# Performance work log

Hardware: AMD Instinct MI355X
Metric: run time of the kernel (lower is better)

## Reference

```python
import jax, jax.numpy as jnp
import numpy as np

N, K, C = 100000, 32, 128  # n_nodes, max_degree, channels


def setup_inputs() -> dict:
    key = jax.random.key(0)
    k1, k2, k3, k4 = jax.random.split(key, 4)
    x = jax.random.normal(k1, (N, C), dtype=jnp.float32)
    edge_index = jax.random.randint(k2, (N, K), 0, N, dtype=jnp.int64)
    # GCNConv uses nn.Linear(in, out, bias=False): weight shape [out, in]
    W1 = jax.random.normal(k3, (C, C), dtype=jnp.float32) / np.sqrt(C)
    W2 = jax.random.normal(k4, (C, C), dtype=jnp.float32) / np.sqrt(C)
    return {"x": x, "edge_index": edge_index, "W1": W1, "W2": W2}


def _gcn_layer(x, edge_index, W):
    # node degree counts valid (>=0) neighbors plus self
    deg = jnp.sum(edge_index >= 0, axis=-1, keepdims=True).astype(x.dtype) + 1.0
    sqrt_deg = jnp.sqrt(deg)
    h = (x @ W.T) / sqrt_deg  # [N, C]
    # pad with a zero row so index -1 (padding) gathers zeros
    padded = jnp.concatenate([h, jnp.zeros((1, h.shape[-1]), h.dtype)], axis=0)
    neigh_sum = padded[edge_index].sum(axis=1)  # [N, K, C] -> [N, C]
    return (neigh_sum + h) / sqrt_deg


def reference(x, edge_index, W1, W2):
    h = jax.nn.elu(_gcn_layer(x, edge_index, W1))
    h = jax.nn.elu(_gcn_layer(h, edge_index, W2))
    return h
```

## Files before the change

### kernel.cpp

```cpp
#include <hip/hip_runtime.h>
#include <hip/hip_bf16.h>
#include <math.h>

namespace {

constexpr int C = 128;
constexpr int K = 32;

typedef float float4v __attribute__((ext_vector_type(4)));
typedef short short8v __attribute__((ext_vector_type(8)));
typedef unsigned short ushort8v __attribute__((ext_vector_type(8)));
typedef int int2v __attribute__((ext_vector_type(2)));

__device__ __forceinline__ float bf2f(unsigned short u) {
    return __uint_as_float(((unsigned int)u) << 16);
}
__device__ __forceinline__ unsigned short f2bf(float x) {
    __hip_bfloat16 h = __float2bfloat16(x);
    return *(unsigned short*)&h;
}

__global__ __launch_bounds__(256) void deg_kernel(
    const int* __restrict__ edge, float* __restrict__ invs,
    unsigned int* __restrict__ hzero, const float* __restrict__ W1,
    const float* __restrict__ W2, unsigned short* __restrict__ whl, int N) {
    const int bid = blockIdx.x;
    const int t = threadIdx.x;

    if (bid == 0 && t < 64) {
        hzero[(size_t)N * (C / 2) + t] = 0u;
    }
    if (bid >= 1 && bid <= 128) {
        int which = (bid - 1) >> 6;
        int p = ((bid - 1) & 63) * 256 + t;
        float w = (which ? W2 : W1)[p];
        unsigned short hb = f2bf(w);
        unsigned short lb = f2bf(w - bf2f(hb));
        unsigned short* dst = whl + (size_t)which * 32768;
        dst[p] = hb;
        dst[16384 + p] = lb;
    }

    int node = bid * 32 + (t >> 3);
    int k4 = (t & 7) * 4;
    int4 e = make_int4(-1, -1, -1, -1);
    if (node < N) e = *(const int4*)(edge + (size_t)node * K + k4);
    int cnt = (e.x >= 0) + (e.y >= 0) + (e.z >= 0) + (e.w >= 0);
    cnt += __shfl_xor(cnt, 1);
    cnt += __shfl_xor(cnt, 2);
    cnt += __shfl_xor(cnt, 4);
    if ((t & 7) == 0 && node < N)
        invs[node] = 1.0f / sqrtf((float)(cnt + 1));
}

__global__ __launch_bounds__(256, 2) void gemm_mfma_kernel(
    const float* __restrict__ X, const unsigned short* __restrict__ Wp,
    const float* __restrict__ invs, unsigned short* __restrict__ H, int N) {
    __shared__ unsigned short Whl[2][C][136];

    const int t = threadIdx.x;
    const int n0 = blockIdx.x * 128;

    for (int p = t; p < 2 * C * 16; p += 256) {
        int seg = p >> 11;
        int rem = p & 2047;
        int row = rem >> 4;
        int v8 = (rem & 15) * 8;
        *(ushort8v*)&Whl[seg][row][v8] =
            *(const ushort8v*)(Wp + (size_t)seg * 16384 + row * 128 + v8);
    }
    __syncthreads();

    const int wv = t >> 6;
    const int l = t & 63;
    const int lm = l & 15;
    const int lk = l >> 4;
    const int rbase = n0 + wv * 32;

    int rowA0 = rbase + lm;
    int rowA1 = rbase + 16 + lm;
    rowA0 = rowA0 < N ? rowA0 : N - 1;
    rowA1 = rowA1 < N ? rowA1 : N - 1;
    const float* xp0 = X + (size_t)rowA0 * C;
    const float* xp1 = X + (size_t)rowA1 * C;

    float4v acc[2][8];
#pragma unroll
    for (int rt = 0; rt < 2; ++rt)
#pragma unroll
        for (int ct = 0; ct < 8; ++ct) acc[rt][ct] = {0.f, 0.f, 0.f, 0.f};

#pragma unroll
    for (int ks = 0; ks < 4; ++ks) {
        const int kb = ks * 32 + lk * 8;
        float xr0[8], xr1[8];
        *(float4v*)&xr0[0] = *(const float4v*)(xp0 + kb);
        *(float4v*)&xr0[4] = *(const float4v*)(xp0 + kb + 4);
        *(float4v*)&xr1[0] = *(const float4v*)(xp1 + kb);
        *(float4v*)&xr1[4] = *(const float4v*)(xp1 + kb + 4);
        short8v ah0, al0, ah1, al1;
#pragma unroll
        for (int j = 0; j < 8; ++j) {
            unsigned short h0 = f2bf(xr0[j]);
            unsigned short h1 = f2bf(xr1[j]);
            ah0[j] = (short)h0;
            ah1[j] = (short)h1;
            al0[j] = (short)f2bf(xr0[j] - bf2f(h0));
            al1[j] = (short)f2bf(xr1[j] - bf2f(h1));
        }
#pragma unroll
        for (int ct = 0; ct < 8; ++ct) {
            short8v bh = *(const short8v*)&Whl[0][ct * 16 + lm][kb];
            short8v bl = *(const short8v*)&Whl[1][ct * 16 + lm][kb];
            acc[0][ct] = __builtin_amdgcn_mfma_f32_16x16x32_bf16(ah0, bh,
                                                                 acc[0][ct], 0, 0, 0);
            acc[0][ct] = __builtin_amdgcn_mfma_f32_16x16x32_bf16(al0, bh,
                                                                 acc[0][ct], 0, 0, 0);
            acc[0][ct] = __builtin_amdgcn_mfma_f32_16x16x32_bf16(ah0, bl,
                                                                 acc[0][ct], 0, 0, 0);
            acc[1][ct] = __builtin_amdgcn_mfma_f32_16x16x32_bf16(ah1, bh,
                                                                 acc[1][ct], 0, 0, 0);
            acc[1][ct] = __builtin_amdgcn_mfma_f32_16x16x32_bf16(al1, bh,
                                                                 acc[1][ct], 0, 0, 0);
            acc[1][ct] = __builtin_amdgcn_mfma_f32_16x16x32_bf16(ah1, bl,
                                                                 acc[1][ct], 0, 0, 0);
        }
    }

    float sc[2][4];
#pragma unroll
    for (int rt = 0; rt < 2; ++rt)
#pragma unroll
        for (int q = 0; q < 4; ++q) {
            int r = rbase + rt * 16 + lk * 4 + q;
            sc[rt][q] = invs[r < N ? r : N - 1];
        }
#pragma unroll
    for (int rt = 0; rt < 2; ++rt)
#pragma unroll
        for (int ct = 0; ct < 8; ++ct)
#pragma unroll
            for (int q = 0; q < 4; ++q) {
                int r = rbase + rt * 16 + lk * 4 + q;
                if (r < N)
                    H[(size_t)r * C + ct * 16 + lm] =
                        f2bf(acc[rt][ct][q] * sc[rt][q]);
            }
}

__global__ __launch_bounds__(256) void gather_elu_kernel(
    const unsigned short* __restrict__ H, const int* __restrict__ edge,
    const float* __restrict__ invs, float* __restrict__ out, int N) {
    __shared__ int idx_s[16][K];

    const int t = threadIdx.x;
    const int g = t >> 4;
    const int l16 = t & 15;
    const int node = blockIdx.x * 16 + g;

    {
        int p = t * 2;
        int r = p >> 5;
        int c0 = p & 31;
        int nn = blockIdx.x * 16 + r;
        int2v e = {-1, -1};
        if (nn < N) e = *(const int2v*)(edge + (size_t)nn * K + c0);
        idx_s[r][c0] = e.x;
        idx_s[r][c0 + 1] = e.y;
    }
    __syncthreads();
    if (node >= N) return;

    const unsigned short* hp = H + l16 * 8;
    float acc[8];
#pragma unroll
    for (int i = 0; i < 8; ++i) acc[i] = 0.f;

#pragma unroll
    for (int k0 = 0; k0 < K; k0 += 16) {
        ushort8v v[16];
#pragma unroll
        for (int u = 0; u < 16; ++u) {
            int j = idx_s[g][k0 + u];
            j = (j < 0) ? N : j;
            v[u] = *(const ushort8v*)(hp + (size_t)j * C);
        }
#pragma unroll
        for (int u = 0; u < 16; ++u)
#pragma unroll
            for (int i = 0; i < 8; ++i) acc[i] += bf2f(v[u][i]);
    }

    ushort8v sv = *(const ushort8v*)(hp + (size_t)node * C);
    float s = invs[node];
    float r[8];
#pragma unroll
    for (int i = 0; i < 8; ++i) {
        float x = (acc[i] + bf2f(sv[i])) * s;
        r[i] = x > 0.f ? x : expm1f(x);
    }
    float* dst = out + (size_t)node * C + l16 * 8;
    float4v lo = {r[0], r[1], r[2], r[3]};
    float4v hi = {r[4], r[5], r[6], r[7]};
    *(float4v*)dst = lo;
    *(float4v*)(dst + 4) = hi;
}

}

extern "C" void kernel_launch(void* const* d_in, const int* in_sizes, int n_in,
                              void* d_out, int out_size, void* d_ws, size_t ws_size,
                              hipStream_t stream) {
    const float* x = (const float*)d_in[0];
    const int* edge = (const int*)d_in[1];
    const float* W1 = (const float*)d_in[2];
    const float* W2 = (const float*)d_in[3];
    float* out = (float*)d_out;
    const int N = in_sizes[0] / C;

    char* ws = (char*)d_ws;
    float* invs = (float*)ws;
    size_t invs_bytes = ((size_t)N * sizeof(float) + 255) & ~(size_t)255;
    unsigned short* h = (unsigned short*)(ws + invs_bytes);
    size_t h_bytes = (((size_t)(N + 1) * C * 2) + 255) & ~(size_t)255;
    unsigned short* whl = (unsigned short*)(ws + invs_bytes + h_bytes);

    const int degBlocks = (N + 31) / 32;
    const int gemmBlocks = (N + 127) / 128;
    const int gatherBlocks = (N + 15) / 16;

    deg_kernel<<<degBlocks, 256, 0, stream>>>(edge, invs, (unsigned int*)h, W1,
                                              W2, whl, N);
    gemm_mfma_kernel<<<gemmBlocks, 256, 0, stream>>>(x, whl, invs, h, N);
    gather_elu_kernel<<<gatherBlocks, 256, 0, stream>>>(h, edge, invs, out, N);
    gemm_mfma_kernel<<<gemmBlocks, 256, 0, stream>>>(out, whl + 32768, invs, h, N);
    gather_elu_kernel<<<gatherBlocks, 256, 0, stream>>>(h, edge, invs, out, N);
}
```

Baseline: 283.4 us.

## Fuse layer-1 gather/ELU with layer-2 GEMM into one kernel

Adds a kernel that gathers neighbor rows, applies ELU, stages the activation tile in shared memory as bf16, and immediately multiplies by W2 via MFMA to produce the layer-2 hidden features. This removes the fp32 intermediate round-trip to global memory and one kernel launch. In exchange, every 16-node block reloads and re-splits the full W2 matrix into shared memory, and the large shared footprint limits occupancy for the latency-bound gather. The activation is also kept as single bf16 rather than a hi/lo split.

```diff
diff --git a/kernel.cpp b/kernel.cpp
--- a/kernel.cpp
+++ b/kernel.cpp
@@ -22,14 +22,14 @@
 
 __global__ __launch_bounds__(256) void deg_kernel(
     const int* __restrict__ edge, float* __restrict__ invs,
-    unsigned int* __restrict__ hzero, const float* __restrict__ W1,
-    const float* __restrict__ W2, unsigned short* __restrict__ whl, int N) {
+    unsigned int* __restrict__ hz1, unsigned int* __restrict__ hz2,
+    const float* __restrict__ W1, const float* __restrict__ W2,
+    unsigned short* __restrict__ whl, int N) {
     const int bid = blockIdx.x;
     const int t = threadIdx.x;
 
-    if (bid == 0 && t < 64) {
-        hzero[(size_t)N * (C / 2) + t] = 0u;
-    }
+    if (bid == 0 && t < 64) hz1[(size_t)N * (C / 2) + t] = 0u;
+    if (bid == 129 && t < 64) hz2[(size_t)N * (C / 2) + t] = 0u;
     if (bid >= 1 && bid <= 128) {
         int which = (bid - 1) >> 6;
         int p = ((bid - 1) & 63) * 256 + t;
@@ -206,6 +206,114 @@
     *(float4v*)(dst + 4) = hi;
 }
 
+__global__ __launch_bounds__(256) void fused_gather_gemm_kernel(
+    const unsigned short* __restrict__ H1, const int* __restrict__ edge,
+    const float* __restrict__ invs, const float* __restrict__ W2,
+    unsigned short* __restrict__ H2, int N) {
+    __shared__ unsigned short Whl[2][C][136];
+    __shared__ unsigned short act_s[16][136];
+    __shared__ int idx_s[16][K];
+
+    const int t = threadIdx.x;
+    const int base = blockIdx.x * 16;
+
+    for (int p = t; p < C * 32; p += 256) {
+        int row = p >> 5;
+        int c4 = (p & 31) * 4;
+        float4 w = ((const float4*)W2)[p];
+        float wv[4] = {w.x, w.y, w.z, w.w};
+#pragma unroll
+        for (int j = 0; j < 4; ++j) {
+            unsigned short hb = f2bf(wv[j]);
+            Whl[0][row][c4 + j] = hb;
+            Whl[1][row][c4 + j] = f2bf(wv[j] - bf2f(hb));
+        }
+    }
+    {
+        int p = t * 2;
+        int r = p >> 5;
+        int c0 = p & 31;
+        int nn = base + r;
+        int2v e = {-1, -1};
+        if (nn < N) e = *(const int2v*)(edge + (size_t)nn * K + c0);
+        idx_s[r][c0] = e.x;
+        idx_s[r][c0 + 1] = e.y;
+    }
+    __syncthreads();
+
+    {
+        const int g = t >> 4;
+        const int l16 = t & 15;
+        const int node = base + g;
+        const unsigned short* hp = H1 + l16 * 8;
+        float acc[8];
+#pragma unroll
+        for (int i = 0; i < 8; ++i) acc[i] = 0.f;
+
+#pragma unroll
+        for (int k0 = 0; k0 < K; k0 += 16) {
+            ushort8v v[16];
+#pragma unroll
+            for (int u = 0; u < 16; ++u) {
+                int j = idx_s[g][k0 + u];
+                j = (j < 0) ? N : j;
+                v[u] = *(const ushort8v*)(hp + (size_t)j * C);
+            }
+#pragma unroll
+            for (int u = 0; u < 16; ++u)
+#pragma unroll
+                for (int i = 0; i < 8; ++i) acc[i] += bf2f(v[u][i]);
+        }
+
+        ushort8v av = {0, 0, 0, 0, 0, 0, 0, 0};
+        if (node < N) {
+            ushort8v sv = *(const ushort8v*)(hp + (size_t)node * C);
+            float s = invs[node];
+#pragma unroll
+            for (int i = 0; i < 8; ++i) {
+                float x = (acc[i] + bf2f(sv[i])) * s;
+                x = x > 0.f ? x : expm1f(x);
+                av[i] = f2bf(x);
+            }
+        }
+        *(ushort8v*)&act_s[g][l16 * 8] = av;
+    }
+    __syncthreads();
+
+    const int wv = t >> 6;
+    const int l = t & 63;
+    const int lm = l & 15;
+    const int lk = l >> 4;
+
+    float4v o[2] = {{0.f, 0.f, 0.f, 0.f}, {0.f, 0.f, 0.f, 0.f}};
+#pragma unroll
+    for (int ks = 0; ks < 4; ++ks) {
+        const int kb = ks * 32 + lk * 8;
+        short8v a = *(const short8v*)&act_s[lm][kb];
+#pragma unroll
+        for (int ci = 0; ci < 2; ++ci) {
+            const int ct = wv * 2 + ci;
+            short8v bh = *(const short8v*)&Whl[0][ct * 16 + lm][kb];
+            short8v bl = *(const short8v*)&Whl[1][ct * 16 + lm][kb];
+            o[ci] = __builtin_amdgcn_mfma_f32_16x16x32_bf16(a, bh, o[ci], 0, 0, 0);
+            o[ci] = __builtin_amdgcn_mfma_f32_16x16x32_bf16(a, bl, o[ci], 0, 0, 0);
+        }
+    }
+
+#pragma unroll
+    for (int q = 0; q < 4; ++q) {
+        const int nd = base + lk * 4 + q;
+        if (nd < N) {
+            float s = invs[nd];
+#pragma unroll
+            for (int ci = 0; ci < 2; ++ci) {
+                H2[(size_t)nd * C + (wv * 2 + ci) * 16 + lm] =
+                    f2bf(o[ci][q] * s);
+            }
+        }
+    }
+}
+
 }
 
 extern "C" void kernel_launch(void* const* d_in, const int* in_sizes, int n_in,
@@ -219,20 +327,36 @@
     const int N = in_sizes[0] / C;
 
     char* ws = (char*)d_ws;
+    const size_t invs_bytes = ((size_t)N * sizeof(float) + 255) & ~(size_t)255;
+    const size_t h_bytes = (((size_t)(N + 1) * C * 2) + 255) & ~(size_t)255;
+    const size_t whl_bytes = 2 * 2 * 16384 * sizeof(unsigned short);
+
     float* invs = (float*)ws;
-    size_t invs_bytes = ((size_t)N * sizeof(float) + 255) & ~(size_t)255;
-    unsigned short* h = (unsigned short*)(ws + invs_bytes);
-    size_t h_bytes = (((size_t)(N + 1) * C * 2) + 255) & ~(size_t)255;
-    unsigned short* whl = (unsigned short*)(ws + invs_bytes + h_bytes);
+    unsigned short* h1 = (unsigned short*)(ws + invs_bytes);
 
     const int degBlocks = (N + 31) / 32;
     const int gemmBlocks = (N + 127) / 128;
     const int gatherBlocks = (N + 15) / 16;
 
-    deg_kernel<<<degBlocks, 256, 0, stream>>>(edge, invs, (unsigned int*)h, W1,
-                                              W2, whl, N);
-    gemm_mfma_kernel<<<gemmBlocks, 256, 0, stream>>>(x, whl, invs, h, N);
-    gather_elu_kernel<<<gatherBlocks, 256, 0, stream>>>(h, edge, invs, out, N);
-    gemm_mfma_kernel<<<gemmBlocks, 256, 0, stream>>>(out, whl + 32768, invs, h, N);
-    gather_elu_kernel<<<gatherBlocks, 256, 0, stream>>>(h, edge, invs, out, N);
-}
+    if (ws_size >= invs_bytes + 2 * h_bytes + whl_bytes) {
+        unsigned short* h2 = (unsigned short*)(ws + invs_bytes + h_bytes);
+        unsigned short* whl = (unsigned short*)(ws + invs_bytes + 2 * h_bytes);
+
+        deg_kernel<<<degBlocks, 256, 0, stream>>>(
+            edge, invs, (unsigned int*)h1, (unsigned int*)h2, W1, W2, whl, N);
+        gemm_mfma_kernel<<<gemmBlocks, 256, 0, stream>>>(x, whl, invs, h1, N);
+        fused_gather_gemm_kernel<<<gatherBlocks, 256, 0, stream>>>(
+            h1, edge, invs, W2, h2, N);
+        gather_elu_kernel<<<gatherBlocks, 256, 0, stream>>>(h2, edge, invs, out, N);
+    } else {
+        unsigned short* whl = (unsigned short*)(ws + invs_bytes + h_bytes);
+
+        deg_kernel<<<degBlocks, 256, 0, stream>>>(
+            edge, invs, (unsigned int*)h1, (unsigned int*)h1, W1, W2, whl, N);
+        gemm_mfma_kernel<<<gemmBlocks, 256, 0, stream>>>(x, whl, invs, h1, N);
+        gather_elu_kernel<<<gatherBlocks, 256, 0, stream>>>(h1, edge, invs, out, N);
+        gemm_mfma_kernel<<<gemmBlocks, 256, 0, stream>>>(out, whl + 32768, invs,
+                                                         h1, N);
+        gather_elu_kernel<<<gatherBlocks, 256, 0, stream>>>(h1, edge, invs, out, N);
+    }
+}
```

Result: slower. 307.8 us (+8.6%).
